# Kernel optimization log

Measured on AMD Instinct MI355X. Metric: run time of the kernel, lower is better.

## Reference

```python
import jax, jax.numpy as jnp
import numpy as np

N_HEAD, D_HEAD, D_MODEL = 8, 64, 512
QLEN, MLEN, BSZ = 1024, 1024, 4
KLEN = QLEN + MLEN
SCALE = 1.0 / (D_HEAD ** 0.5)
LN_EPS = 1e-5


def _rel_shift(x):
    # x: [qlen, rlen, bsz, n_head]
    q, rl, b, n = x.shape
    zero_pad = jnp.zeros((q, 1, b, n), x.dtype)
    x_padded = jnp.concatenate([zero_pad, x], axis=1).reshape(rl + 1, q, b, n)
    return x_padded[1:].reshape(q, rl, b, n)


def _layer_norm(x, g, b):
    mu = jnp.mean(x, axis=-1, keepdims=True)
    var = jnp.var(x, axis=-1, keepdims=True)
    return (x - mu) * jax.lax.rsqrt(var + LN_EPS) * g + b


def setup_inputs() -> dict:
    key = jax.random.key(0)
    ks = jax.random.split(key, 10)
    s = 0.02
    return {
        "w": jax.random.normal(ks[0], (QLEN, BSZ, D_MODEL), jnp.float32),
        "r": jax.random.normal(ks[1], (KLEN, 1, D_MODEL), jnp.float32),
        "r_w_bias": jax.random.normal(ks[2], (N_HEAD, D_HEAD), jnp.float32) * s,
        "r_r_bias": jax.random.normal(ks[3], (N_HEAD, D_HEAD), jnp.float32) * s,
        "mems": jax.random.normal(ks[4], (MLEN, BSZ, D_MODEL), jnp.float32),
        "Wq": jax.random.normal(ks[5], (D_MODEL, N_HEAD * D_HEAD), jnp.float32) * s,
        "Wkv": jax.random.normal(ks[6], (D_MODEL, 2 * N_HEAD * D_HEAD), jnp.float32) * s,
        "Wr": jax.random.normal(ks[7], (D_MODEL, N_HEAD * D_HEAD), jnp.float32) * s,
        "Wo": jax.random.normal(ks[8], (N_HEAD * D_HEAD, D_MODEL), jnp.float32) * s,
        "ln_g": jnp.ones((D_MODEL,), jnp.float32),
        "ln_b": jnp.zeros((D_MODEL,), jnp.float32),
        # causal mask: query i can attend keys j <= i + MLEN
        "attn_mask": jnp.arange(KLEN)[None, :] > (jnp.arange(QLEN) + MLEN)[:, None],
    }


def reference(w, r, r_w_bias, r_r_bias, mems, Wq, Wkv, Wr, Wo, ln_g, ln_b, attn_mask):
    qlen, bsz = w.shape[0], w.shape[1]
    cat = jnp.concatenate([mems, w], axis=0)          # [klen, bsz, d_model]
    klen = cat.shape[0]

    r_head_k = (r[:, 0] @ Wr).reshape(-1, N_HEAD, D_HEAD)   # [rlen, n, d]
    kv = cat @ Wkv                                           # [klen, bsz, 2*n*d]
    w_head_k, w_head_v = jnp.split(kv, 2, axis=-1)
    w_head_q = (cat[-qlen:] @ Wq).reshape(qlen, bsz, N_HEAD, D_HEAD)
    w_head_k = w_head_k.reshape(klen, bsz, N_HEAD, D_HEAD)
    w_head_v = w_head_v.reshape(klen, bsz, N_HEAD, D_HEAD)

    AC = jnp.einsum('ibnd,jbnd->ijbn', w_head_q + r_w_bias, w_head_k)
    BD = jnp.einsum('ibnd,jnd->ijbn', w_head_q + r_r_bias, r_head_k)
    BD = _rel_shift(BD)[:, :klen]

    attn_score = (AC + BD) * SCALE                           # [qlen, klen, bsz, n]
    attn_score = jnp.where(attn_mask[:, :, None, None], -jnp.inf, attn_score)
    attn_prob = jax.nn.softmax(attn_score, axis=1)

    attn_vec = jnp.einsum('ijbn,jbnd->ibnd', attn_prob, w_head_v)
    attn_vec = attn_vec.reshape(qlen, bsz, N_HEAD * D_HEAD)
    attn_out = attn_vec @ Wo
    return _layer_norm(w + attn_out, ln_g, ln_b)
```

## Files before the change

kernel.cpp:

```cpp
#include <hip/hip_runtime.h>
#include <hip/hip_bf16.h>
#include <math.h>

#define QLEN 1024
#define MLEN 1024
#define KLEN 2048
#define BSZ 4
#define NH 8
#define DH 64
#define DM 512
#define SCALE 0.125f
#define LN_EPS 1e-5f

#define RK_ROWS 2112

typedef __attribute__((ext_vector_type(8))) short short8;
typedef __attribute__((ext_vector_type(4))) float float4_;

#define GLB(p) ((const __attribute__((address_space(1))) void*)(p))
#define LDSP(p) ((__attribute__((address_space(3))) void*)(p))

__device__ inline ushort to_bf16(float x) {
  __hip_bfloat16 h = __float2bfloat16(x);
  return *reinterpret_cast<ushort*>(&h);
}

__device__ inline float row_max16(float v) {
  int x = __builtin_bit_cast(int, v);
  v = fmaxf(v, __builtin_bit_cast(float, __builtin_amdgcn_update_dpp(x, x, 0xB1, 0xF, 0xF, false)));
  x = __builtin_bit_cast(int, v);
  v = fmaxf(v, __builtin_bit_cast(float, __builtin_amdgcn_update_dpp(x, x, 0x4E, 0xF, 0xF, false)));
  x = __builtin_bit_cast(int, v);
  v = fmaxf(v, __builtin_bit_cast(float, __builtin_amdgcn_update_dpp(x, x, 0x124, 0xF, 0xF, false)));
  x = __builtin_bit_cast(int, v);
  v = fmaxf(v, __builtin_bit_cast(float, __builtin_amdgcn_update_dpp(x, x, 0x128, 0xF, 0xF, false)));
  return v;
}
__device__ inline float row_sum16(float v) {
  int x = __builtin_bit_cast(int, v);
  v += __builtin_bit_cast(float, __builtin_amdgcn_update_dpp(x, x, 0xB1, 0xF, 0xF, false));
  x = __builtin_bit_cast(int, v);
  v += __builtin_bit_cast(float, __builtin_amdgcn_update_dpp(x, x, 0x4E, 0xF, 0xF, false));
  x = __builtin_bit_cast(int, v);
  v += __builtin_bit_cast(float, __builtin_amdgcn_update_dpp(x, x, 0x124, 0xF, 0xF, false));
  x = __builtin_bit_cast(int, v);
  v += __builtin_bit_cast(float, __builtin_amdgcn_update_dpp(x, x, 0x128, 0xF, 0xF, false));
  return v;
}

__global__ __launch_bounds__(256) void wtrans_all(
    const float* __restrict__ Wq, const float* __restrict__ Wkv,
    const float* __restrict__ Wr, const float* __restrict__ Wo,
    ushort* __restrict__ WqT, ushort* __restrict__ WkvT,
    ushort* __restrict__ WrT, ushort* __restrict__ WoT) {
  __shared__ ushort tile[32][33];
  const int z = blockIdx.z;
  const float* W;
  ushort* WT;
  int N;
  if (z == 0)      { W = Wq;  WT = WqT;  N = DM; }
  else if (z == 1) { W = Wkv; WT = WkvT; N = 2 * DM; }
  else if (z == 2) { W = Wr;  WT = WrT;  N = DM; }
  else             { W = Wo;  WT = WoT;  N = DM; }
  const int k0 = blockIdx.x * 32, n0 = blockIdx.y * 32;
  if (n0 >= N) return;
  const int tid = threadIdx.x;
#pragma unroll
  for (int it = 0; it < 4; ++it) {
    int idx = tid + it * 256;
    int r = idx >> 5, c = idx & 31;
    tile[r][c] = to_bf16(W[(size_t)(k0 + r) * N + n0 + c]);
  }
  __syncthreads();
#pragma unroll
  for (int it = 0; it < 4; ++it) {
    int idx = tid + it * 256;
    int r = idx >> 5, c = idx & 31;
    WT[(size_t)(n0 + r) * DM + k0 + c] = tile[c][r];
  }
}

__global__ __launch_bounds__(256) void proj_all(
    const float* __restrict__ w, const float* __restrict__ mems,
    const float* __restrict__ r,
    const ushort* __restrict__ WqT, const ushort* __restrict__ WkvT,
    const ushort* __restrict__ WrT,
    const float* __restrict__ bias0, const float* __restrict__ bias1,
    ushort* __restrict__ qw, ushort* __restrict__ qr,
    ushort* __restrict__ k2, ushort* __restrict__ v2,
    ushort* __restrict__ rk2) {
  __shared__ ushort As[128 * 32];
  __shared__ ushort Bs[128 * 32];
  const int tid = threadIdx.x;
  int mode, bx, by;
  {
    int id = blockIdx.x;
    if (id < 128)      { mode = 0; bx = id >> 2;         by = id & 3; }
    else if (id < 640) { mode = 1; bx = (id - 128) >> 3; by = (id - 128) & 7; }
    else               { mode = 2; bx = (id - 640) >> 2; by = (id - 640) & 3; }
  }
  const int m0 = bx * 128, n0 = by * 128;
  const int wv = tid >> 6, lane = tid & 63;
  const int wm = wv >> 1, wn = wv & 1;
  const int l16 = lane & 15, quad = lane >> 4;

  const int arow = tid >> 1;
  const int acol = (tid & 1) * 16;
  const float* asrc;
  {
    int m = m0 + arow;
    if (mode == 2) asrc = r + (size_t)m * DM;
    else asrc = (m < QLEN * BSZ) ? w + (size_t)m * DM
                                 : mems + (size_t)(m - QLEN * BSZ) * DM;
    asrc += acol;
  }
  const ushort* BT = (mode == 0) ? WqT : (mode == 1) ? WkvT : WrT;
  const ushort* bsrc = BT + (size_t)(n0 + arow) * DM + acol;

  float4_ acc[4][4];
#pragma unroll
  for (int a = 0; a < 4; ++a)
#pragma unroll
    for (int b = 0; b < 4; ++b) acc[a][b] = float4_{0.f, 0.f, 0.f, 0.f};

  for (int k0 = 0; k0 < DM; k0 += 32) {
    float4 a0 = *reinterpret_cast<const float4*>(asrc + k0);
    float4 a1 = *reinterpret_cast<const float4*>(asrc + k0 + 4);
    float4 a2 = *reinterpret_cast<const float4*>(asrc + k0 + 8);
    float4 a3 = *reinterpret_cast<const float4*>(asrc + k0 + 12);
    ushort4 u0, u1, u2, u3;
    u0.x = to_bf16(a0.x); u0.y = to_bf16(a0.y); u0.z = to_bf16(a0.z); u0.w = to_bf16(a0.w);
    u1.x = to_bf16(a1.x); u1.y = to_bf16(a1.y); u1.z = to_bf16(a1.z); u1.w = to_bf16(a1.w);
    u2.x = to_bf16(a2.x); u2.y = to_bf16(a2.y); u2.z = to_bf16(a2.z); u2.w = to_bf16(a2.w);
    u3.x = to_bf16(a3.x); u3.y = to_bf16(a3.y); u3.z = to_bf16(a3.z); u3.w = to_bf16(a3.w);
    *reinterpret_cast<ushort4*>(&As[arow * 32 + acol]) = u0;
    *reinterpret_cast<ushort4*>(&As[arow * 32 + acol + 4]) = u1;
    *reinterpret_cast<ushort4*>(&As[arow * 32 + acol + 8]) = u2;
    *reinterpret_cast<ushort4*>(&As[arow * 32 + acol + 12]) = u3;
    *reinterpret_cast<uint4*>(&Bs[arow * 32 + acol]) =
        *reinterpret_cast<const uint4*>(bsrc + k0);
    *reinterpret_cast<uint4*>(&Bs[arow * 32 + acol + 8]) =
        *reinterpret_cast<const uint4*>(bsrc + k0 + 8);
    __syncthreads();
    short8 af[4], bf[4];
#pragma unroll
    for (int f = 0; f < 4; ++f) {
      af[f] = *reinterpret_cast<const short8*>(&As[(wm * 64 + f * 16 + l16) * 32 + quad * 8]);
      bf[f] = *reinterpret_cast<const short8*>(&Bs[(wn * 64 + f * 16 + l16) * 32 + quad * 8]);
    }
#pragma unroll
    for (int fm = 0; fm < 4; ++fm)
#pragma unroll
      for (int fn = 0; fn < 4; ++fn)
        acc[fm][fn] = __builtin_amdgcn_mfma_f32_16x16x32_bf16(bf[fn], af[fm], acc[fm][fn], 0, 0, 0);
    __syncthreads();
  }

#pragma unroll
  for (int fm = 0; fm < 4; ++fm) {
#pragma unroll
    for (int fn = 0; fn < 4; ++fn) {
      const int mm = m0 + wm * 64 + fm * 16 + l16;
      const int nnb = n0 + wn * 64 + fn * 16 + quad * 4;
      const float4_ a = acc[fm][fn];
      if (mode == 0) {
        float4 b0v = *reinterpret_cast<const float4*>(bias0 + nnb);
        float4 b1v = *reinterpret_cast<const float4*>(bias1 + nnb);
        int i = mm >> 2, b = mm & 3;
        int hd = nnb >> 6, d0 = nnb & 63;
        size_t idx = (((size_t)(b * NH + hd)) * QLEN + i) * DH + d0;
        ushort4 o0, o1;
        o0.x = to_bf16(a[0] + b0v.x); o0.y = to_bf16(a[1] + b0v.y);
        o0.z = to_bf16(a[2] + b0v.z); o0.w = to_bf16(a[3] + b0v.w);
        o1.x = to_bf16(a[0] + b1v.x); o1.y = to_bf16(a[1] + b1v.y);
        o1.z = to_bf16(a[2] + b1v.z); o1.w = to_bf16(a[3] + b1v.w);
        *reinterpret_cast<ushort4*>(qw + idx) = o0;
        *reinterpret_cast<ushort4*>(qr + idx) = o1;
      } else if (mode == 1) {
        int pos = mm >> 2, b = mm & 3;
        int jb = pos >> 5, jj = pos & 31;
        if (nnb < DM) {
          int hd = nnb >> 6, d = nnb & 63;
          int bn = b * NH + hd;
          int tile = ((jj >> 4) << 1) | (d >> 5);
          int lane2 = (((d >> 3) & 3) << 4) | (jj & 15);
          ushort4 o;
          o.x = to_bf16(a[0]); o.y = to_bf16(a[1]);
          o.z = to_bf16(a[2]); o.w = to_bf16(a[3]);
          *reinterpret_cast<ushort4*>(
              k2 + ((((size_t)bn * 64 + jb) * 4 + tile) * 64 + lane2) * 8 + (d & 7)) = o;
        } else {
          int nn2 = nnb - DM;
          int hd = nn2 >> 6, d = nn2 & 63;
          int bn = b * NH + hd;
          int tile = d >> 4;
          size_t base = ((((size_t)bn * 64 + jb) * 4 + tile) * 64 +
                         ((jj >> 3) << 4)) * 8 + (jj & 7);
#pragma unroll
          for (int reg = 0; reg < 4; ++reg)
            v2[base + (size_t)((d & 15) + reg) * 8] = to_bf16(a[reg]);
        }
      } else {
        int t = mm;
        int hd = nnb >> 6, d = nnb & 63;
        int cb = d >> 3;
        int dcol = ((cb ^ (t & 7)) << 3) | (d & 7);
        ushort4 o;
        o.x = to_bf16(a[0]); o.y = to_bf16(a[1]);
        o.z = to_bf16(a[2]); o.w = to_bf16(a[3]);
        *reinterpret_cast<ushort4*>(
            rk2 + ((size_t)hd * RK_ROWS + t) * DH + dcol) = o;
      }
    }
  }
}

__global__ __launch_bounds__(256) void mfma_out(
    const ushort* __restrict__ A, const ushort* __restrict__ BT,
    float* __restrict__ Y) {
  __shared__ ushort As[128 * 32];
  __shared__ ushort Bs[128 * 32];
  const int tid = threadIdx.x;
  const int m0 = blockIdx.x * 128, n0 = blockIdx.y * 128;
  const int wv = tid >> 6, lane = tid & 63;
  const int wm = wv >> 1, wn = wv & 1;
  const int l16 = lane & 15, quad = lane >> 4;
  const int arow = tid >> 1;
  const int acol = (tid & 1) * 16;
  const ushort* asrc = A + (size_t)(m0 + arow) * DM + acol;
  const ushort* bsrc = BT + (size_t)(n0 + arow) * DM + acol;

  float4_ acc[4][4];
#pragma unroll
  for (int a = 0; a < 4; ++a)
#pragma unroll
    for (int b = 0; b < 4; ++b) acc[a][b] = float4_{0.f, 0.f, 0.f, 0.f};

  for (int k0 = 0; k0 < DM; k0 += 32) {
    *reinterpret_cast<uint4*>(&As[arow * 32 + acol]) = *reinterpret_cast<const uint4*>(asrc + k0);
    *reinterpret_cast<uint4*>(&As[arow * 32 + acol + 8]) = *reinterpret_cast<const uint4*>(asrc + k0 + 8);
    *reinterpret_cast<uint4*>(&Bs[arow * 32 + acol]) = *reinterpret_cast<const uint4*>(bsrc + k0);
    *reinterpret_cast<uint4*>(&Bs[arow * 32 + acol + 8]) = *reinterpret_cast<const uint4*>(bsrc + k0 + 8);
    __syncthreads();
    short8 af[4], bf[4];
#pragma unroll
    for (int f = 0; f < 4; ++f) {
      af[f] = *reinterpret_cast<const short8*>(&As[(wm * 64 + f * 16 + l16) * 32 + quad * 8]);
      bf[f] = *reinterpret_cast<const short8*>(&Bs[(wn * 64 + f * 16 + l16) * 32 + quad * 8]);
    }
#pragma unroll
    for (int fm = 0; fm < 4; ++fm)
#pragma unroll
      for (int fn = 0; fn < 4; ++fn)
        acc[fm][fn] = __builtin_amdgcn_mfma_f32_16x16x32_bf16(bf[fn], af[fm], acc[fm][fn], 0, 0, 0);
    __syncthreads();
  }
#pragma unroll
  for (int fm = 0; fm < 4; ++fm)
#pragma unroll
    for (int fn = 0; fn < 4; ++fn) {
      int mm = m0 + wm * 64 + fm * 16 + l16;
      int nnb = n0 + wn * 64 + fn * 16 + quad * 4;
      float4 o;
      o.x = acc[fm][fn][0]; o.y = acc[fm][fn][1];
      o.z = acc[fm][fn][2]; o.w = acc[fm][fn][3];
      *reinterpret_cast<float4*>(Y + (size_t)mm * DM + nnb) = o;
    }
}

__global__ __launch_bounds__(256) void ln_fuse(
    const float* __restrict__ y, const float* __restrict__ wres,
    const float* __restrict__ g, const float* __restrict__ bb,
    float* __restrict__ out) {
  const int row = blockIdx.x * 4 + (threadIdx.x >> 6);
  const int lane = threadIdx.x & 63;
  const float* yr = y + (size_t)row * DM + lane * 4;
  const float* wr = wres + (size_t)row * DM + lane * 4;
  float4 x0 = *(const float4*)yr;
  float4 x1 = *(const float4*)(yr + 256);
  float4 w0 = *(const float4*)wr;
  float4 w1 = *(const float4*)(wr + 256);
  x0.x += w0.x; x0.y += w0.y; x0.z += w0.z; x0.w += w0.w;
  x1.x += w1.x; x1.y += w1.y; x1.z += w1.z; x1.w += w1.w;
  float s = x0.x + x0.y + x0.z + x0.w + x1.x + x1.y + x1.z + x1.w;
  float ss = x0.x * x0.x + x0.y * x0.y + x0.z * x0.z + x0.w * x0.w +
             x1.x * x1.x + x1.y * x1.y + x1.z * x1.z + x1.w * x1.w;
#pragma unroll
  for (int off = 1; off <= 32; off <<= 1) {
    s += __shfl_xor(s, off, 64);
    ss += __shfl_xor(ss, off, 64);
  }
  float mu = s * (1.f / DM);
  float var = ss * (1.f / DM) - mu * mu;
  float rstd = rsqrtf(var + LN_EPS);
  float4 g0 = *(const float4*)(g + lane * 4);
  float4 g1 = *(const float4*)(g + lane * 4 + 256);
  float4 b0 = *(const float4*)(bb + lane * 4);
  float4 b1 = *(const float4*)(bb + lane * 4 + 256);
  float4 o0, o1;
  o0.x = (x0.x - mu) * rstd * g0.x + b0.x;
  o0.y = (x0.y - mu) * rstd * g0.y + b0.y;
  o0.z = (x0.z - mu) * rstd * g0.z + b0.z;
  o0.w = (x0.w - mu) * rstd * g0.w + b0.w;
  o1.x = (x1.x - mu) * rstd * g1.x + b1.x;
  o1.y = (x1.y - mu) * rstd * g1.y + b1.y;
  o1.z = (x1.z - mu) * rstd * g1.z + b1.z;
  o1.w = (x1.w - mu) * rstd * g1.w + b1.w;
  float* orow = out + (size_t)row * DM + lane * 4;
  *reinterpret_cast<float4*>(orow) = o0;
  *reinterpret_cast<float4*>(orow + 256) = o1;
}

__global__ __launch_bounds__(256) void attn_mfma(
    const ushort* __restrict__ qw, const ushort* __restrict__ qr,
    const ushort* __restrict__ k2, const ushort* __restrict__ v2,
    const ushort* __restrict__ rk2, ushort* __restrict__ avbf) {
  const int i0b = (gridDim.x - 1 - blockIdx.x) * 64;
  const int n = blockIdx.y, b = blockIdx.z;
  const int bn = b * NH + n;
  const int tid = threadIdx.x;
  const int wv = tid >> 6, lane = tid & 63;
  const int l16 = lane & 15, quad = lane >> 4;
  const int i0w = i0b + wv * 16;

  __shared__ ushort stage[2][20 * 512];
  __shared__ float Dlds[4][16 * 66];
  __shared__ ushort Plds[4][16 * 32];
  float* __restrict__ Dw = Dlds[wv];
  ushort* __restrict__ Pw = Plds[wv];

  const ushort* __restrict__ k2b = k2 + (size_t)bn * (64 * 4 * 512);
  const ushort* __restrict__ v2b = v2 + (size_t)bn * (64 * 4 * 512);
  const ushort* __restrict__ rk2n = rk2 + (size_t)n * RK_ROWS * DH;

  const int nIter = (i0b + 63 + MLEN) / 32 + 1;

  short8 aqw0, aqw1, aqr0, aqr1;
  {
    const ushort* qwp = qw + (((size_t)bn * QLEN) + i0w + l16) * DH + quad * 8;
    const ushort* qrp = qr + (((size_t)bn * QLEN) + i0w + l16) * DH + quad * 8;
    aqw0 = *(const short8*)(qwp);
    aqw1 = *(const short8*)(qwp + 32);
    aqr0 = *(const short8*)(qrp);
    aqr1 = *(const short8*)(qrp + 32);
  }

  auto issue_dma = [&](int jb, int buf) {
    const int tbase = jb * 32 - i0b + 960;
#pragma unroll
    for (int s = 0; s < 5; ++s) {
      const int m = wv + s * 4;
      const ushort* g;
      if (m < 8) {
        const ushort* base = (m < 4) ? k2b : v2b;
        g = base + ((size_t)jb * 4 + (m & 3)) * 512 + lane * 8;
      } else {
        int tr = tbase + (m - 8) * 8 + (lane >> 3);
        g = rk2n + (size_t)tr * DH + (lane & 7) * 8;
      }
      __builtin_amdgcn_global_load_lds(GLB(g), LDSP(&stage[buf][m * 512]), 16, 0, 0);
    }
  };

  float4_ O[4];
#pragma unroll
  for (int t = 0; t < 4; ++t) O[t] = float4_{0.f, 0.f, 0.f, 0.f};
  float mrow[4] = {-INFINITY, -INFINITY, -INFINITY, -INFINITY};
  float lpart[4] = {0.f, 0.f, 0.f, 0.f};
  const float SL2E = SCALE * 1.44269504088896f;
  const int rbase = 48 - 16 * wv;
  const int sw = (l16 & 7);

  issue_dma(0, 0);
  issue_dma(1 < nIter ? 1 : 0, 1);

  for (int k = 0; k < nIter; ++k) {
    __builtin_amdgcn_s_waitcnt(0x0F75);
    __builtin_amdgcn_sched_barrier(0);
    __builtin_amdgcn_s_barrier();
    __builtin_amdgcn_sched_barrier(0);
    const ushort* sb = stage[k & 1];
    const int j0 = k * 32;

    float4_ ac[2];
#pragma unroll
    for (int h = 0; h < 2; ++h) {
      short8 b0 = *(const short8*)(sb + (h * 2 + 0) * 512 + lane * 8);
      short8 b1 = *(const short8*)(sb + (h * 2 + 1) * 512 + lane * 8);
      float4_ c = {0.f, 0.f, 0.f, 0.f};
      c = __builtin_amdgcn_mfma_f32_16x16x32_bf16(aqw0, b0, c, 0, 0, 0);
      c = __builtin_amdgcn_mfma_f32_16x16x32_bf16(aqw1, b1, c, 0, 0, 0);
      ac[h] = c;
    }
#pragma unroll
    for (int tt = 0; tt < 3; ++tt) {
      int rowLoc = rbase + tt * 16 + l16;
      const ushort* rrow = sb + 4096 + rowLoc * 64;
      short8 b0 = *(const short8*)(rrow + (((0 + quad) ^ sw) << 3));
      short8 b1 = *(const short8*)(rrow + (((4 + quad) ^ sw) << 3));
      float4_ d = {0.f, 0.f, 0.f, 0.f};
      d = __builtin_amdgcn_mfma_f32_16x16x32_bf16(aqr0, b0, d, 0, 0, 0);
      d = __builtin_amdgcn_mfma_f32_16x16x32_bf16(aqr1, b1, d, 0, 0, 0);
#pragma unroll
      for (int rg = 0; rg < 4; ++rg) {
        int row = quad * 4 + rg;
        Dw[row * 66 + tt * 16 + l16 + row] = d[rg];
      }
    }
    float s[2][4];
#pragma unroll
    for (int half = 0; half < 2; ++half) {
#pragma unroll
      for (int rg = 0; rg < 4; ++rg) {
        int row = quad * 4 + rg;
        int jloc = half * 16 + l16;
        float bd = Dw[row * 66 + jloc + 15];
        float sv = (ac[half][rg] + bd) * SL2E;
        s[half][rg] = (j0 + jloc > i0w + row + MLEN) ? -INFINITY : sv;
      }
    }
#pragma unroll
    for (int rg = 0; rg < 4; ++rg) {
      float mx = row_max16(fmaxf(s[0][rg], s[1][rg]));
      float mn = fmaxf(mrow[rg], mx);
      float alpha = __builtin_amdgcn_exp2f(mrow[rg] - mn);
      float p0 = __builtin_amdgcn_exp2f(s[0][rg] - mn);
      float p1 = __builtin_amdgcn_exp2f(s[1][rg] - mn);
      lpart[rg] = lpart[rg] * alpha + (p0 + p1);
      mrow[rg] = mn;
#pragma unroll
      for (int t = 0; t < 4; ++t) O[t][rg] *= alpha;
      int row = quad * 4 + rg;
      int idx0 = (l16 >> 3) * 128 + row * 8 + (l16 & 7);
      Pw[idx0] = to_bf16(p0);
      Pw[idx0 + 256] = to_bf16(p1);
    }
    short8 pfrag = *(const short8*)(Pw + lane * 8);
#pragma unroll
    for (int t = 0; t < 4; ++t) {
      short8 vfrag = *(const short8*)(sb + (4 + t) * 512 + lane * 8);
      O[t] = __builtin_amdgcn_mfma_f32_16x16x32_bf16(pfrag, vfrag, O[t], 0, 0, 0);
    }

    __builtin_amdgcn_sched_barrier(0);
    __builtin_amdgcn_s_barrier();
    __builtin_amdgcn_sched_barrier(0);
    int jn = k + 2;
    if (jn > nIter - 1) jn = nIter - 1;
    issue_dma(jn, k & 1);
  }

  float inv[4];
#pragma unroll
  for (int rg = 0; rg < 4; ++rg) inv[rg] = 1.f / row_sum16(lpart[rg]);
#pragma unroll
  for (int t = 0; t < 4; ++t)
#pragma unroll
    for (int rg = 0; rg < 4; ++rg) {
      int row = quad * 4 + rg;
      avbf[((size_t)(i0w + row) * BSZ + b) * DM + n * DH + t * 16 + l16] =
          to_bf16(O[t][rg] * inv[rg]);
    }
}

extern "C" void kernel_launch(void* const* d_in, const int* in_sizes, int n_in,
                              void* d_out, int out_size, void* d_ws, size_t ws_size,
                              hipStream_t stream) {
  const float* w    = (const float*)d_in[0];
  const float* r    = (const float*)d_in[1];
  const float* rwb  = (const float*)d_in[2];
  const float* rrb  = (const float*)d_in[3];
  const float* mems = (const float*)d_in[4];
  const float* Wq   = (const float*)d_in[5];
  const float* Wkv  = (const float*)d_in[6];
  const float* Wr   = (const float*)d_in[7];
  const float* Wo   = (const float*)d_in[8];
  const float* ln_g = (const float*)d_in[9];
  const float* ln_b = (const float*)d_in[10];
  float* out = (float*)d_out;

  char* p = (char*)d_ws;
  auto alloc = [&](size_t bytes) {
    char* q = p;
    p += (bytes + 255) & ~(size_t)255;
    return q;
  };
  ushort* WqT   = (ushort*)alloc((size_t)DM * DM * 2);
  ushort* WkvT  = (ushort*)alloc((size_t)2 * DM * DM * 2);
  ushort* WrT   = (ushort*)alloc((size_t)DM * DM * 2);
  ushort* WoT   = (ushort*)alloc((size_t)DM * DM * 2);
  ushort* qw    = (ushort*)alloc((size_t)BSZ * NH * QLEN * DH * 2);
  ushort* qr    = (ushort*)alloc((size_t)BSZ * NH * QLEN * DH * 2);
  ushort* k2    = (ushort*)alloc((size_t)BSZ * NH * 64 * 4 * 512 * 2);
  ushort* v2    = (ushort*)alloc((size_t)BSZ * NH * 64 * 4 * 512 * 2);
  ushort* rk2   = (ushort*)alloc((size_t)NH * RK_ROWS * DH * 2);
  ushort* avbf  = (ushort*)alloc((size_t)QLEN * BSZ * DM * 2);
  float* y = (float*)k2;

  wtrans_all<<<dim3(16, 32, 4), dim3(256), 0, stream>>>(
      Wq, Wkv, Wr, Wo, WqT, WkvT, WrT, WoT);
  proj_all<<<dim3(704), dim3(256), 0, stream>>>(
      w, mems, r, WqT, WkvT, WrT, rwb, rrb, qw, qr, k2, v2, rk2);
  attn_mfma<<<dim3(QLEN / 64, NH, BSZ), dim3(256), 0, stream>>>(qw, qr, k2, v2, rk2, avbf);
  mfma_out<<<dim3(32, 4), dim3(256), 0, stream>>>(avbf, WoT, y);
  ln_fuse<<<dim3(QLEN * BSZ / 4), dim3(256), 0, stream>>>(y, w, ln_g, ln_b, out);
}
```

Measured before the change: 252.4 us.

## Fuse output projection with layernorm and stage V-projection writes through LDS

Replaces the separate Wo GEMM and layernorm kernels with one kernel in which each block computes a full 16-row strip of the output projection, then applies the residual add and layernorm in registers, removing the fp32 intermediate round-trip and one launch. The V-projection epilogue in proj_all now transposes tiles through a swizzled shared-memory buffer so that its global stores are 16-byte coalesced, replacing the scattered 2-byte writes. The fused kernel reads WoT directly from global memory with no LDS reuse across blocks and has smaller tiles, so it relies on cache hits for the weight reads.

New measurement: 260.8 us. 3.3% more time.

```diff
diff --git a/kernel.cpp b/kernel.cpp
--- a/kernel.cpp
+++ b/kernel.cpp
@@ -89,8 +89,9 @@
     ushort* __restrict__ qw, ushort* __restrict__ qr,
     ushort* __restrict__ k2, ushort* __restrict__ v2,
     ushort* __restrict__ rk2) {
-  __shared__ ushort As[128 * 32];
-  __shared__ ushort Bs[128 * 32];
+  __shared__ ushort smem[128 * 68];
+  ushort* As = smem;
+  ushort* Bs = smem + 128 * 32;
   const int tid = threadIdx.x;
   int mode, bx, by;
   {
@@ -156,6 +157,51 @@
     __syncthreads();
   }
 
+  if (mode == 1 && n0 >= DM) {
+    const int jb = bx;
+    const int hd0 = (n0 - DM) >> 6;
+#pragma unroll
+    for (int pass = 0; pass < 2; ++pass) {
+      if (wn == pass) {
+#pragma unroll
+        for (int fm = 0; fm < 4; ++fm)
+#pragma unroll
+          for (int fn = 0; fn < 4; ++fn) {
+            int row = wm * 64 + fm * 16 + l16;
+            int col4 = fn * 4 + quad;
+            int c4s = col4 ^ (row >> 5);
+            const float4_ a = acc[fm][fn];
+            ushort4 o;
+            o.x = to_bf16(a[0]); o.y = to_bf16(a[1]);
+            o.z = to_bf16(a[2]); o.w = to_bf16(a[3]);
+            *reinterpret_cast<ushort4*>(&smem[row * 68 + c4s * 4]) = o;
+          }
+      }
+      __syncthreads();
+      {
+        const int b = tid >> 6;
+        const int lane2 = tid & 63;
+        const int octet = (lane2 >> 4) & 3;
+        const int bn = b * NH + hd0 + pass;
+        ushort* chunk = v2 + (((size_t)bn * 64 + jb) * 4) * 512;
+#pragma unroll
+        for (int s = 0; s < 4; ++s) {
+          const int d = s * 16 + (lane2 & 15);
+          const int c4s = (d >> 2) ^ octet;
+          const int cl = c4s * 4 + (d & 3);
+          ushort val[8];
+#pragma unroll
+          for (int u = 0; u < 8; ++u)
+            val[u] = smem[((octet * 8 + u) * 4 + b) * 68 + cl];
+          *reinterpret_cast<uint4*>(chunk + (size_t)s * 512 + lane2 * 8) =
+              *reinterpret_cast<uint4*>(val);
+        }
+      }
+      __syncthreads();
+    }
+    return;
+  }
+
 #pragma unroll
   for (int fm = 0; fm < 4; ++fm) {
 #pragma unroll
@@ -179,27 +225,15 @@
       } else if (mode == 1) {
         int pos = mm >> 2, b = mm & 3;
         int jb = pos >> 5, jj = pos & 31;
-        if (nnb < DM) {
-          int hd = nnb >> 6, d = nnb & 63;
-          int bn = b * NH + hd;
-          int tile = ((jj >> 4) << 1) | (d >> 5);
-          int lane2 = (((d >> 3) & 3) << 4) | (jj & 15);
-          ushort4 o;
-          o.x = to_bf16(a[0]); o.y = to_bf16(a[1]);
-          o.z = to_bf16(a[2]); o.w = to_bf16(a[3]);
-          *reinterpret_cast<ushort4*>(
-              k2 + ((((size_t)bn * 64 + jb) * 4 + tile) * 64 + lane2) * 8 + (d & 7)) = o;
-        } else {
-          int nn2 = nnb - DM;
-          int hd = nn2 >> 6, d = nn2 & 63;
-          int bn = b * NH + hd;
-          int tile = d >> 4;
-          size_t base = ((((size_t)bn * 64 + jb) * 4 + tile) * 64 +
-                         ((jj >> 3) << 4)) * 8 + (jj & 7);
-#pragma unroll
-          for (int reg = 0; reg < 4; ++reg)
-            v2[base + (size_t)((d & 15) + reg) * 8] = to_bf16(a[reg]);
-        }
+        int hd = nnb >> 6, d = nnb & 63;
+        int bn = b * NH + hd;
+        int tile = ((jj >> 4) << 1) | (d >> 5);
+        int lane2 = (((d >> 3) & 3) << 4) | (jj & 15);
+        ushort4 o;
+        o.x = to_bf16(a[0]); o.y = to_bf16(a[1]);
+        o.z = to_bf16(a[2]); o.w = to_bf16(a[3]);
+        *reinterpret_cast<ushort4*>(
+            k2 + ((((size_t)bn * 64 + jb) * 4 + tile) * 64 + lane2) * 8 + (d & 7)) = o;
       } else {
         int t = mm;
         int hd = nnb >> 6, d = nnb & 63;
@@ -215,100 +249,72 @@
   }
 }
 
-__global__ __launch_bounds__(256) void mfma_out(
-    const ushort* __restrict__ A, const ushort* __restrict__ BT,
-    float* __restrict__ Y) {
-  __shared__ ushort As[128 * 32];
-  __shared__ ushort Bs[128 * 32];
+__global__ __launch_bounds__(256) void out_ln_mfma(
+    const ushort* __restrict__ avbf, const ushort* __restrict__ WoT,
+    const float* __restrict__ wres, const float* __restrict__ g,
+    const float* __restrict__ bb, float* __restrict__ out) {
+  __shared__ ushort As[16 * 32];
+  __shared__ float red[2][4][16];
   const int tid = threadIdx.x;
-  const int m0 = blockIdx.x * 128, n0 = blockIdx.y * 128;
   const int wv = tid >> 6, lane = tid & 63;
-  const int wm = wv >> 1, wn = wv & 1;
   const int l16 = lane & 15, quad = lane >> 4;
-  const int arow = tid >> 1;
-  const int acol = (tid & 1) * 16;
-  const ushort* asrc = A + (size_t)(m0 + arow) * DM + acol;
-  const ushort* bsrc = BT + (size_t)(n0 + arow) * DM + acol;
-
-  float4_ acc[4][4];
-#pragma unroll
-  for (int a = 0; a < 4; ++a)
-#pragma unroll
-    for (int b = 0; b < 4; ++b) acc[a][b] = float4_{0.f, 0.f, 0.f, 0.f};
+  const int m0 = blockIdx.x * 16;
+
+  float4_ acc[8];
+#pragma unroll
+  for (int f = 0; f < 8; ++f) acc[f] = float4_{0.f, 0.f, 0.f, 0.f};
 
   for (int k0 = 0; k0 < DM; k0 += 32) {
-    *reinterpret_cast<uint4*>(&As[arow * 32 + acol]) = *reinterpret_cast<const uint4*>(asrc + k0);
-    *reinterpret_cast<uint4*>(&As[arow * 32 + acol + 8]) = *reinterpret_cast<const uint4*>(asrc + k0 + 8);
-    *reinterpret_cast<uint4*>(&Bs[arow * 32 + acol]) = *reinterpret_cast<const uint4*>(bsrc + k0);
-    *reinterpret_cast<uint4*>(&Bs[arow * 32 + acol + 8]) = *reinterpret_cast<const uint4*>(bsrc + k0 + 8);
+    if (tid < 128)
+      *reinterpret_cast<ushort4*>(&As[(tid >> 3) * 32 + (tid & 7) * 4]) =
+          *reinterpret_cast<const ushort4*>(
+              avbf + (size_t)(m0 + (tid >> 3)) * DM + k0 + (tid & 7) * 4);
     __syncthreads();
-    short8 af[4], bf[4];
-#pragma unroll
-    for (int f = 0; f < 4; ++f) {
-      af[f] = *reinterpret_cast<const short8*>(&As[(wm * 64 + f * 16 + l16) * 32 + quad * 8]);
-      bf[f] = *reinterpret_cast<const short8*>(&Bs[(wn * 64 + f * 16 + l16) * 32 + quad * 8]);
-    }
-#pragma unroll
-    for (int fm = 0; fm < 4; ++fm)
-#pragma unroll
-      for (int fn = 0; fn < 4; ++fn)
-        acc[fm][fn] = __builtin_amdgcn_mfma_f32_16x16x32_bf16(bf[fn], af[fm], acc[fm][fn], 0, 0, 0);
+    short8 af = *reinterpret_cast<const short8*>(&As[l16 * 32 + quad * 8]);
+#pragma unroll
+    for (int fn = 0; fn < 8; ++fn) {
+      short8 bf = *reinterpret_cast<const short8*>(
+          WoT + (size_t)(wv * 128 + fn * 16 + l16) * DM + k0 + quad * 8);
+      acc[fn] = __builtin_amdgcn_mfma_f32_16x16x32_bf16(bf, af, acc[fn], 0, 0, 0);
+    }
     __syncthreads();
   }
-#pragma unroll
-  for (int fm = 0; fm < 4; ++fm)
-#pragma unroll
-    for (int fn = 0; fn < 4; ++fn) {
-      int mm = m0 + wm * 64 + fm * 16 + l16;
-      int nnb = n0 + wn * 64 + fn * 16 + quad * 4;
-      float4 o;
-      o.x = acc[fm][fn][0]; o.y = acc[fm][fn][1];
-      o.z = acc[fm][fn][2]; o.w = acc[fm][fn][3];
-      *reinterpret_cast<float4*>(Y + (size_t)mm * DM + nnb) = o;
-    }
-}
-
-__global__ __launch_bounds__(256) void ln_fuse(
-    const float* __restrict__ y, const float* __restrict__ wres,
-    const float* __restrict__ g, const float* __restrict__ bb,
-    float* __restrict__ out) {
-  const int row = blockIdx.x * 4 + (threadIdx.x >> 6);
-  const int lane = threadIdx.x & 63;
-  const float* yr = y + (size_t)row * DM + lane * 4;
-  const float* wr = wres + (size_t)row * DM + lane * 4;
-  float4 x0 = *(const float4*)yr;
-  float4 x1 = *(const float4*)(yr + 256);
-  float4 w0 = *(const float4*)wr;
-  float4 w1 = *(const float4*)(wr + 256);
-  x0.x += w0.x; x0.y += w0.y; x0.z += w0.z; x0.w += w0.w;
-  x1.x += w1.x; x1.y += w1.y; x1.z += w1.z; x1.w += w1.w;
-  float s = x0.x + x0.y + x0.z + x0.w + x1.x + x1.y + x1.z + x1.w;
-  float ss = x0.x * x0.x + x0.y * x0.y + x0.z * x0.z + x0.w * x0.w +
-             x1.x * x1.x + x1.y * x1.y + x1.z * x1.z + x1.w * x1.w;
-#pragma unroll
-  for (int off = 1; off <= 32; off <<= 1) {
-    s += __shfl_xor(s, off, 64);
-    ss += __shfl_xor(ss, off, 64);
-  }
-  float mu = s * (1.f / DM);
-  float var = ss * (1.f / DM) - mu * mu;
+
+  const int row = m0 + l16;
+  float s = 0.f, ss = 0.f;
+  float4 xv[8];
+#pragma unroll
+  for (int fn = 0; fn < 8; ++fn) {
+    int ncol = wv * 128 + fn * 16 + quad * 4;
+    float4 wv4 = *reinterpret_cast<const float4*>(wres + (size_t)row * DM + ncol);
+    float4 x;
+    x.x = acc[fn][0] + wv4.x; x.y = acc[fn][1] + wv4.y;
+    x.z = acc[fn][2] + wv4.z; x.w = acc[fn][3] + wv4.w;
+    xv[fn] = x;
+    s += x.x + x.y + x.z + x.w;
+    ss += x.x * x.x + x.y * x.y + x.z * x.z + x.w * x.w;
+  }
+  s += __shfl_xor(s, 16, 64);  s += __shfl_xor(s, 32, 64);
+  ss += __shfl_xor(ss, 16, 64); ss += __shfl_xor(ss, 32, 64);
+  if (quad == 0) { red[0][wv][l16] = s; red[1][wv][l16] = ss; }
+  __syncthreads();
+  float S = red[0][0][l16] + red[0][1][l16] + red[0][2][l16] + red[0][3][l16];
+  float SS = red[1][0][l16] + red[1][1][l16] + red[1][2][l16] + red[1][3][l16];
+  float mu = S * (1.f / DM);
+  float var = SS * (1.f / DM) - mu * mu;
   float rstd = rsqrtf(var + LN_EPS);
-  float4 g0 = *(const float4*)(g + lane * 4);
-  float4 g1 = *(const float4*)(g + lane * 4 + 256);
-  float4 b0 = *(const float4*)(bb + lane * 4);
-  float4 b1 = *(const float4*)(bb + lane * 4 + 256);
-  float4 o0, o1;
-  o0.x = (x0.x - mu) * rstd * g0.x + b0.x;
-  o0.y = (x0.y - mu) * rstd * g0.y + b0.y;
-  o0.z = (x0.z - mu) * rstd * g0.z + b0.z;
-  o0.w = (x0.w - mu) * rstd * g0.w + b0.w;
-  o1.x = (x1.x - mu) * rstd * g1.x + b1.x;
-  o1.y = (x1.y - mu) * rstd * g1.y + b1.y;
-  o1.z = (x1.z - mu) * rstd * g1.z + b1.z;
-  o1.w = (x1.w - mu) * rstd * g1.w + b1.w;
-  float* orow = out + (size_t)row * DM + lane * 4;
-  *reinterpret_cast<float4*>(orow) = o0;
-  *reinterpret_cast<float4*>(orow + 256) = o1;
+#pragma unroll
+  for (int fn = 0; fn < 8; ++fn) {
+    int ncol = wv * 128 + fn * 16 + quad * 4;
+    float4 g4 = *reinterpret_cast<const float4*>(g + ncol);
+    float4 b4 = *reinterpret_cast<const float4*>(bb + ncol);
+    float4 o;
+    o.x = (xv[fn].x - mu) * rstd * g4.x + b4.x;
+    o.y = (xv[fn].y - mu) * rstd * g4.y + b4.y;
+    o.z = (xv[fn].z - mu) * rstd * g4.z + b4.z;
+    o.w = (xv[fn].w - mu) * rstd * g4.w + b4.w;
+    *reinterpret_cast<float4*>(out + (size_t)row * DM + ncol) = o;
+  }
 }
 
 __global__ __launch_bounds__(256) void attn_mfma(
@@ -495,13 +501,12 @@
   ushort* v2    = (ushort*)alloc((size_t)BSZ * NH * 64 * 4 * 512 * 2);
   ushort* rk2   = (ushort*)alloc((size_t)NH * RK_ROWS * DH * 2);
   ushort* avbf  = (ushort*)alloc((size_t)QLEN * BSZ * DM * 2);
-  float* y = (float*)k2;
 
   wtrans_all<<<dim3(16, 32, 4), dim3(256), 0, stream>>>(
       Wq, Wkv, Wr, Wo, WqT, WkvT, WrT, WoT);
   proj_all<<<dim3(704), dim3(256), 0, stream>>>(
       w, mems, r, WqT, WkvT, WrT, rwb, rrb, qw, qr, k2, v2, rk2);
   attn_mfma<<<dim3(QLEN / 64, NH, BSZ), dim3(256), 0, stream>>>(qw, qr, k2, v2, rk2, avbf);
-  mfma_out<<<dim3(32, 4), dim3(256), 0, stream>>>(avbf, WoT, y);
-  ln_fuse<<<dim3(QLEN * BSZ / 4), dim3(256), 0, stream>>>(y, w, ln_g, ln_b, out);
-}
+  out_ln_mfma<<<dim3(QLEN * BSZ / 16), dim3(256), 0, stream>>>(
+      avbf, WoT, w, ln_g, ln_b, out);
+}
```
